# Kernel tuning notes

Hardware: AMD Instinct MI355X
Metric: run time of the kernel (lower is better)

The kernel has to match this reference:

```python
import jax, jax.numpy as jnp
import numpy as np

BATCH = 16384
N_FEATURES = 768
FT_OUT = 1024
ACTIVE_P = 32.0 / 768.0  # ~32 active features per board, like real positions


def setup_inputs() -> dict:
    key = jax.random.key(0)
    k1, k2, k3, k4, k5, k6 = jax.random.split(key, 6)
    # densified sparse one-hot boards: binary {0,1} with ~32/768 density
    board_stm = (jax.random.uniform(k1, (BATCH, N_FEATURES)) < ACTIVE_P).astype(jnp.float32)
    board_nstm = (jax.random.uniform(k2, (BATCH, N_FEATURES)) < ACTIVE_P).astype(jnp.float32)
    # Linear(768, FT_OUT): weight [out, in], bias [out]
    W_ft = jax.random.normal(k3, (FT_OUT, N_FEATURES), dtype=jnp.float32) * (1.0 / np.sqrt(N_FEATURES))
    b_ft = jax.random.normal(k4, (FT_OUT,), dtype=jnp.float32) * 0.01
    # Linear(2*FT_OUT, 1)
    W_out = jax.random.normal(k5, (1, 2 * FT_OUT), dtype=jnp.float32) * (1.0 / np.sqrt(2 * FT_OUT))
    b_out = jax.random.normal(k6, (1,), dtype=jnp.float32) * 0.01
    return {"board_stm": board_stm, "board_nstm": board_nstm,
            "W_ft": W_ft, "b_ft": b_ft, "W_out": W_out, "b_out": b_out}


def screlu(x):
    # SCReLU: clamp(x, 0, 1)^2
    return jnp.square(jnp.clip(x, 0.0, 1.0))


def reference(board_stm, board_nstm, W_ft, b_ft, W_out, b_out):
    # feature transformer applied to both perspectives (shared weights)
    stm = jnp.einsum('bf,of->bo', board_stm, W_ft) + b_ft   # [B, FT_OUT]
    nstm = jnp.einsum('bf,of->bo', board_nstm, W_ft) + b_ft  # [B, FT_OUT]
    hidden = screlu(jnp.concatenate([stm, nstm], axis=1))    # [B, 2*FT_OUT]
    out = jnp.einsum('bh,oh->bo', hidden, W_out) + b_out     # [B, 1]
    return jax.nn.sigmoid(out)
```

## Files before the change

### kernel.cpp

```cpp
#include <hip/hip_runtime.h>
#include <stdint.h>

#define BATCH 16384
#define NF 768
#define FT 1024
#define RB 32
#define GR 64
#define THREADS 1024
#define NW 16
#define NKS 12
#define ABLK (NKS * 4 * 64 * 16)

typedef int i32x4 __attribute__((ext_vector_type(4)));

__global__ __launch_bounds__(192) void prep_wq(const float* __restrict__ W_ft,
                                               char* __restrict__ Wq,
                                               float* __restrict__ invs) {
    const int o = blockIdx.x;
    const int t = threadIdx.x;
    __shared__ float smax[3];
    __shared__ float sscale;
    const float4 v = *(const float4*)(W_ft + (size_t)o * NF + t * 4);
    float m = fmaxf(fmaxf(fabsf(v.x), fabsf(v.y)), fmaxf(fabsf(v.z), fabsf(v.w)));
    #pragma unroll
    for (int s = 32; s > 0; s >>= 1) m = fmaxf(m, __shfl_down(m, s, 64));
    if ((t & 63) == 0) smax[t >> 6] = m;
    __syncthreads();
    if (t == 0) {
        const float am = fmaxf(fmaxf(smax[0], smax[1]), smax[2]);
        sscale = 127.0f / am;
        invs[o] = am / 127.0f;
    }
    __syncthreads();
    const float s = sscale;
    const float arr[4] = {v.x, v.y, v.z, v.w};
    uint32_t pk = 0;
    #pragma unroll
    for (int j = 0; j < 4; ++j) {
        const int q = (int)rintf(arr[j] * s);
        pk |= ((uint32_t)(unsigned char)(char)q) << (8 * j);
    }
    *(uint32_t*)(Wq + (size_t)o * NF + t * 4) = pk;
}

__device__ __forceinline__ uint32_t pack01(float4 v) {
    return (uint32_t)(v.x != 0.0f) | ((uint32_t)(v.y != 0.0f) << 8)
         | ((uint32_t)(v.z != 0.0f) << 16) | ((uint32_t)(v.w != 0.0f) << 24);
}

__device__ __forceinline__ int frag_slot(int row, int c16) {
    const int r = row >> 4, cl = row & 15;
    const int ks = c16 >> 2, q = c16 & 3;
    return ((ks * 4 + r) << 6) + q * 16 + cl;
}

__global__ __launch_bounds__(256) void conv_boards(const float* __restrict__ bstm,
                                                   const float* __restrict__ bnstm,
                                                   unsigned char* __restrict__ a8f) {
    const int NCH = BATCH * 48;
    for (int g = blockIdx.x * 256 + threadIdx.x; g < 2 * NCH; g += gridDim.x * 256) {
        const int p = (g >= NCH);
        const int gg = p ? g - NCH : g;
        const int brow = gg / 48;
        const int c16 = gg - brow * 48;
        const float4* src = (const float4*)((p ? bnstm : bstm)
                                            + (size_t)brow * NF + c16 * 16);
        uint4 o;
        o.x = pack01(src[0]); o.y = pack01(src[1]);
        o.z = pack01(src[2]); o.w = pack01(src[3]);
        const int blk = brow >> 5;
        const int row = (p << 5) | (brow & 31);
        *(uint4*)(a8f + (size_t)blk * ABLK + ((size_t)frag_slot(row, c16) << 4)) = o;
    }
}

template <bool PRE8>
__global__ __launch_bounds__(THREADS, 2) void nnue_mfma(
    const float* __restrict__ bstm, const float* __restrict__ bnstm,
    const unsigned char* __restrict__ a8f,
    const char* __restrict__ Wq, const float* __restrict__ invs,
    const float* __restrict__ b_ft, const float* __restrict__ W_out,
    const float* __restrict__ b_out, float* __restrict__ out)
{
    __shared__ __align__(16) char Albs[ABLK];
    __shared__ float red[GR][NW];

    const int t = threadIdx.x;
    const int w = t >> 6;
    const int l = t & 63;
    const int b0 = blockIdx.x * RB;

    if (PRE8) {
        const uint4* src = (const uint4*)(a8f + (size_t)blockIdx.x * ABLK);
        uint4* dst = (uint4*)Albs;
        const uint4 v0 = src[t], v1 = src[1024 + t], v2 = src[2048 + t];
        dst[t] = v0; dst[1024 + t] = v1; dst[2048 + t] = v2;
    } else {
        #pragma unroll
        for (int it = 0; it < 3; ++it) {
            const int c = it * 1024 + t;
            const int row = c / 48;
            const int c16 = c - row * 48;
            const float4* s = (const float4*)(((row < RB)
                ? (bstm + (size_t)(b0 + row) * NF)
                : (bnstm + (size_t)(b0 + row - RB) * NF)) + c16 * 16);
            uint4 o;
            o.x = pack01(s[0]); o.y = pack01(s[1]);
            o.z = pack01(s[2]); o.w = pack01(s[3]);
            *(uint4*)(Albs + ((size_t)frag_slot(row, c16) << 4)) = o;
        }
    }
    __syncthreads();

    const int cl = l & 15;
    const char* bp = Wq + (size_t)(w * 64 + cl) * NF + (l >> 4) * 16;
    const i32x4* af = (const i32x4*)Albs;

    i32x4 be[4], bo[4];
    #pragma unroll
    for (int c = 0; c < 4; ++c)
        be[c] = *(const i32x4*)(bp + (size_t)c * 16 * NF);

    i32x4 acc[4][4] = {};
    #pragma unroll
    for (int kk = 0; kk < 6; ++kk) {
        const int ks0 = 2 * kk, ks1 = 2 * kk + 1;
        #pragma unroll
        for (int c = 0; c < 4; ++c)
            bo[c] = *(const i32x4*)(bp + (size_t)c * 16 * NF + ks1 * 64);
        __builtin_amdgcn_s_setprio(1);
        #pragma unroll
        for (int r = 0; r < 4; ++r) {
            const i32x4 a = af[(ks0 * 4 + r) * 64 + l];
            #pragma unroll
            for (int c = 0; c < 4; ++c)
                acc[r][c] = __builtin_amdgcn_mfma_i32_16x16x64_i8(
                    a, be[c], acc[r][c], 0, 0, 0);
        }
        __builtin_amdgcn_s_setprio(0);
        if (kk < 5) {
            #pragma unroll
            for (int c = 0; c < 4; ++c)
                be[c] = *(const i32x4*)(bp + (size_t)c * 16 * NF + (ks1 + 1) * 64);
        }
        __builtin_amdgcn_s_setprio(1);
        #pragma unroll
        for (int r = 0; r < 4; ++r) {
            const i32x4 a = af[(ks1 * 4 + r) * 64 + l];
            #pragma unroll
            for (int c = 0; c < 4; ++c)
                acc[r][c] = __builtin_amdgcn_mfma_i32_16x16x64_i8(
                    a, bo[c], acc[r][c], 0, 0, 0);
        }
        __builtin_amdgcn_s_setprio(0);
    }

    const int q = l >> 4;
    float ps[4][4] = {};
    #pragma unroll
    for (int c = 0; c < 4; ++c) {
        const int col = w * 64 + c * 16 + cl;
        const float iv = invs[col];
        const float bf = b_ft[col];
        const float wo0 = W_out[col];
        const float wo1 = W_out[FT + col];
        #pragma unroll
        for (int r = 0; r < 4; ++r) {
            const float wo = (r < 2) ? wo0 : wo1;
            #pragma unroll
            for (int j = 0; j < 4; ++j) {
                float h = fmaf((float)acc[r][c][j], iv, bf);
                h = fminf(fmaxf(h, 0.0f), 1.0f);
                ps[r][j] = fmaf(h * h, wo, ps[r][j]);
            }
        }
    }
    #pragma unroll
    for (int r = 0; r < 4; ++r)
        #pragma unroll
        for (int j = 0; j < 4; ++j) {
            float v = ps[r][j];
            v += __shfl_xor(v, 1, 64);
            v += __shfl_xor(v, 2, 64);
            v += __shfl_xor(v, 4, 64);
            v += __shfl_xor(v, 8, 64);
            if (cl == 0) red[16 * r + 4 * q + j][w] = v;
        }
    __syncthreads();

    if (t < RB) {
        float x = b_out[0];
        #pragma unroll
        for (int w2 = 0; w2 < NW; ++w2)
            x += red[t][w2] + red[RB + t][w2];
        out[b0 + t] = 1.0f / (1.0f + expf(-x));
    }
}

extern "C" void kernel_launch(void* const* d_in, const int* in_sizes, int n_in,
                              void* d_out, int out_size, void* d_ws, size_t ws_size,
                              hipStream_t stream) {
    const float* board_stm  = (const float*)d_in[0];
    const float* board_nstm = (const float*)d_in[1];
    const float* W_ft       = (const float*)d_in[2];
    const float* b_ft       = (const float*)d_in[3];
    const float* W_out      = (const float*)d_in[4];
    const float* b_out      = (const float*)d_in[5];
    float* out = (float*)d_out;

    char* Wq = (char*)d_ws;
    float* invs = (float*)((char*)d_ws + (size_t)FT * NF);
    unsigned char* a8f = (unsigned char*)d_ws + (size_t)FT * NF + 4096;
    const size_t needed = (size_t)FT * NF + 4096 + (size_t)(BATCH / RB) * ABLK;

    prep_wq<<<FT, 192, 0, stream>>>(W_ft, Wq, invs);
    if (ws_size >= needed) {
        conv_boards<<<2048, 256, 0, stream>>>(board_stm, board_nstm, a8f);
        nnue_mfma<true><<<BATCH / RB, THREADS, 0, stream>>>(
            board_stm, board_nstm, a8f, Wq, invs, b_ft, W_out, b_out, out);
    } else {
        nnue_mfma<false><<<BATCH / RB, THREADS, 0, stream>>>(
            board_stm, board_nstm, a8f, Wq, invs, b_ft, W_out, b_out, out);
    }
}
```

Before: 86.31 us.

## Retile MFMA kernel to 64-board blocks split across two column halves

Drops the separate board-packing pre-pass and packs boards into LDS inside the main kernel, using batched float4 loads ahead of a sched barrier. Each block now handles 64 boards (128 A rows) with 512 threads, covering half of the feature-transformer columns. Partial sums from the two column halves go to a workspace buffer, and a small finalize kernel adds them and applies the sigmoid. The intent is to remove the extra global round trip for packed boards and double A reuse per weight load. The cost is that each board is read by two blocks, plus one extra launch and higher register pressure from 8x4 accumulators.

```diff
diff --git a/kernel.cpp b/kernel.cpp
--- a/kernel.cpp
+++ b/kernel.cpp
@@ -4,12 +4,14 @@
 #define BATCH 16384
 #define NF 768
 #define FT 1024
-#define RB 32
-#define GR 64
-#define THREADS 1024
-#define NW 16
+#define RBB 64
+#define GR 128
+#define NRF 8
+#define THREADS 512
+#define NWAVE 8
 #define NKS 12
-#define ABLK (NKS * 4 * 64 * 16)
+#define CH_COLS 512
+#define ABLK (NKS * NRF * 64 * 16)
 
 typedef int i32x4 __attribute__((ext_vector_type(4)));
 
@@ -48,72 +50,56 @@
          | ((uint32_t)(v.z != 0.0f) << 16) | ((uint32_t)(v.w != 0.0f) << 24);
 }
 
-__device__ __forceinline__ int frag_slot(int row, int c16) {
-    const int r = row >> 4, cl = row & 15;
-    const int ks = c16 >> 2, q = c16 & 3;
-    return ((ks * 4 + r) << 6) + q * 16 + cl;
-}
-
-__global__ __launch_bounds__(256) void conv_boards(const float* __restrict__ bstm,
-                                                   const float* __restrict__ bnstm,
-                                                   unsigned char* __restrict__ a8f) {
-    const int NCH = BATCH * 48;
-    for (int g = blockIdx.x * 256 + threadIdx.x; g < 2 * NCH; g += gridDim.x * 256) {
-        const int p = (g >= NCH);
-        const int gg = p ? g - NCH : g;
-        const int brow = gg / 48;
-        const int c16 = gg - brow * 48;
-        const float4* src = (const float4*)((p ? bnstm : bstm)
-                                            + (size_t)brow * NF + c16 * 16);
-        uint4 o;
-        o.x = pack01(src[0]); o.y = pack01(src[1]);
-        o.z = pack01(src[2]); o.w = pack01(src[3]);
-        const int blk = brow >> 5;
-        const int row = (p << 5) | (brow & 31);
-        *(uint4*)(a8f + (size_t)blk * ABLK + ((size_t)frag_slot(row, c16) << 4)) = o;
-    }
-}
-
-template <bool PRE8>
 __global__ __launch_bounds__(THREADS, 2) void nnue_mfma(
     const float* __restrict__ bstm, const float* __restrict__ bnstm,
-    const unsigned char* __restrict__ a8f,
     const char* __restrict__ Wq, const float* __restrict__ invs,
     const float* __restrict__ b_ft, const float* __restrict__ W_out,
-    const float* __restrict__ b_out, float* __restrict__ out)
+    float* __restrict__ pbuf)
 {
     __shared__ __align__(16) char Albs[ABLK];
-    __shared__ float red[GR][NW];
+    __shared__ float red[GR][NWAVE];
 
     const int t = threadIdx.x;
     const int w = t >> 6;
     const int l = t & 63;
-    const int b0 = blockIdx.x * RB;
-
-    if (PRE8) {
-        const uint4* src = (const uint4*)(a8f + (size_t)blockIdx.x * ABLK);
-        uint4* dst = (uint4*)Albs;
-        const uint4 v0 = src[t], v1 = src[1024 + t], v2 = src[2048 + t];
-        dst[t] = v0; dst[1024 + t] = v1; dst[2048 + t] = v2;
-    } else {
-        #pragma unroll
-        for (int it = 0; it < 3; ++it) {
-            const int c = it * 1024 + t;
-            const int row = c / 48;
-            const int c16 = c - row * 48;
-            const float4* s = (const float4*)(((row < RB)
-                ? (bstm + (size_t)(b0 + row) * NF)
-                : (bnstm + (size_t)(b0 + row - RB) * NF)) + c16 * 16);
-            uint4 o;
-            o.x = pack01(s[0]); o.y = pack01(s[1]);
-            o.z = pack01(s[2]); o.w = pack01(s[3]);
-            *(uint4*)(Albs + ((size_t)frag_slot(row, c16) << 4)) = o;
+    const int rg = blockIdx.x >> 1;
+    const int ch = blockIdx.x & 1;
+
+    {
+        const int srow = t & 127;
+        const int tq = t >> 7;
+        const int r = srow >> 4, cl = srow & 15;
+        const float* abase = (srow < RBB)
+            ? (bstm + (size_t)(rg * RBB + srow) * NF)
+            : (bnstm + (size_t)(rg * RBB + srow - RBB) * NF);
+        #pragma unroll
+        for (int bt = 0; bt < 3; ++bt) {
+            float4 v[16];
+            #pragma unroll
+            for (int cc = 0; cc < 4; ++cc) {
+                const int c16 = tq + 4 * (bt * 4 + cc);
+                #pragma unroll
+                for (int u = 0; u < 4; ++u)
+                    v[cc * 4 + u] = *(const float4*)(abase + c16 * 16 + u * 4);
+            }
+            __builtin_amdgcn_sched_barrier(0);
+            #pragma unroll
+            for (int cc = 0; cc < 4; ++cc) {
+                const int c16 = tq + 4 * (bt * 4 + cc);
+                const int ks = c16 >> 2, q = c16 & 3;
+                uint4 o;
+                o.x = pack01(v[cc * 4 + 0]); o.y = pack01(v[cc * 4 + 1]);
+                o.z = pack01(v[cc * 4 + 2]); o.w = pack01(v[cc * 4 + 3]);
+                const int slot = ((ks * NRF + r) << 6) + (q << 4) + cl;
+                *(uint4*)(&Albs[(size_t)slot << 4]) = o;
+            }
         }
     }
     __syncthreads();
 
     const int cl = l & 15;
-    const char* bp = Wq + (size_t)(w * 64 + cl) * NF + (l >> 4) * 16;
+    const int q = l >> 4;
+    const char* bp = Wq + (size_t)(ch * CH_COLS + w * 64 + cl) * NF + q * 16;
     const i32x4* af = (const i32x4*)Albs;
 
     i32x4 be[4], bo[4];
@@ -121,7 +107,7 @@
     for (int c = 0; c < 4; ++c)
         be[c] = *(const i32x4*)(bp + (size_t)c * 16 * NF);
 
-    i32x4 acc[4][4] = {};
+    i32x4 acc[NRF][4] = {};
     #pragma unroll
     for (int kk = 0; kk < 6; ++kk) {
         const int ks0 = 2 * kk, ks1 = 2 * kk + 1;
@@ -130,8 +116,8 @@
             bo[c] = *(const i32x4*)(bp + (size_t)c * 16 * NF + ks1 * 64);
         __builtin_amdgcn_s_setprio(1);
         #pragma unroll
-        for (int r = 0; r < 4; ++r) {
-            const i32x4 a = af[(ks0 * 4 + r) * 64 + l];
+        for (int r = 0; r < NRF; ++r) {
+            const i32x4 a = af[(ks0 * NRF + r) * 64 + l];
             #pragma unroll
             for (int c = 0; c < 4; ++c)
                 acc[r][c] = __builtin_amdgcn_mfma_i32_16x16x64_i8(
@@ -145,8 +131,8 @@
         }
         __builtin_amdgcn_s_setprio(1);
         #pragma unroll
-        for (int r = 0; r < 4; ++r) {
-            const i32x4 a = af[(ks1 * 4 + r) * 64 + l];
+        for (int r = 0; r < NRF; ++r) {
+            const i32x4 a = af[(ks1 * NRF + r) * 64 + l];
             #pragma unroll
             for (int c = 0; c < 4; ++c)
                 acc[r][c] = __builtin_amdgcn_mfma_i32_16x16x64_i8(
@@ -155,18 +141,17 @@
         __builtin_amdgcn_s_setprio(0);
     }
 
-    const int q = l >> 4;
-    float ps[4][4] = {};
+    float ps[NRF][4] = {};
     #pragma unroll
     for (int c = 0; c < 4; ++c) {
-        const int col = w * 64 + c * 16 + cl;
+        const int col = ch * CH_COLS + w * 64 + c * 16 + cl;
         const float iv = invs[col];
         const float bf = b_ft[col];
         const float wo0 = W_out[col];
         const float wo1 = W_out[FT + col];
         #pragma unroll
-        for (int r = 0; r < 4; ++r) {
-            const float wo = (r < 2) ? wo0 : wo1;
+        for (int r = 0; r < NRF; ++r) {
+            const float wo = (r < 4) ? wo0 : wo1;
             #pragma unroll
             for (int j = 0; j < 4; ++j) {
                 float h = fmaf((float)acc[r][c][j], iv, bf);
@@ -176,7 +161,7 @@
         }
     }
     #pragma unroll
-    for (int r = 0; r < 4; ++r)
+    for (int r = 0; r < NRF; ++r)
         #pragma unroll
         for (int j = 0; j < 4; ++j) {
             float v = ps[r][j];
@@ -188,13 +173,21 @@
         }
     __syncthreads();
 
-    if (t < RB) {
-        float x = b_out[0];
-        #pragma unroll
-        for (int w2 = 0; w2 < NW; ++w2)
-            x += red[t][w2] + red[RB + t][w2];
-        out[b0 + t] = 1.0f / (1.0f + expf(-x));
-    }
+    if (t < RBB) {
+        float x = 0.0f;
+        #pragma unroll
+        for (int w2 = 0; w2 < NWAVE; ++w2)
+            x += red[t][w2] + red[RBB + t][w2];
+        pbuf[(size_t)ch * BATCH + rg * RBB + t] = x;
+    }
+}
+
+__global__ __launch_bounds__(256) void finalize(const float* __restrict__ pbuf,
+                                                const float* __restrict__ b_out,
+                                                float* __restrict__ out) {
+    const int i = blockIdx.x * 256 + threadIdx.x;
+    const float x = pbuf[i] + pbuf[BATCH + i] + b_out[0];
+    out[i] = 1.0f / (1.0f + expf(-x));
 }
 
 extern "C" void kernel_launch(void* const* d_in, const int* in_sizes, int n_in,
@@ -210,16 +203,10 @@
 
     char* Wq = (char*)d_ws;
     float* invs = (float*)((char*)d_ws + (size_t)FT * NF);
-    unsigned char* a8f = (unsigned char*)d_ws + (size_t)FT * NF + 4096;
-    const size_t needed = (size_t)FT * NF + 4096 + (size_t)(BATCH / RB) * ABLK;
+    float* pbuf = (float*)((char*)d_ws + (size_t)FT * NF + 4096);
 
     prep_wq<<<FT, 192, 0, stream>>>(W_ft, Wq, invs);
-    if (ws_size >= needed) {
-        conv_boards<<<2048, 256, 0, stream>>>(board_stm, board_nstm, a8f);
-        nnue_mfma<true><<<BATCH / RB, THREADS, 0, stream>>>(
-            board_stm, board_nstm, a8f, Wq, invs, b_ft, W_out, b_out, out);
-    } else {
-        nnue_mfma<false><<<BATCH / RB, THREADS, 0, stream>>>(
-            board_stm, board_nstm, a8f, Wq, invs, b_ft, W_out, b_out, out);
-    }
-}
+    nnue_mfma<<<(BATCH / RBB) * 2, THREADS, 0, stream>>>(
+        board_stm, board_nstm, Wq, invs, b_ft, W_out, pbuf);
+    finalize<<<BATCH / 256, 256, 0, stream>>>(pbuf, b_out, out);
+}
```

Measured after the change: 78.86 us. -8.6%, faster.
